# Optimization experiments

Hardware: AMD Instinct MI355X
Metric: run time of the kernel (lower is better)

The kernel has to match this reference:

```python
import jax, jax.numpy as jnp
import numpy as np

NU, NI = 100000, 50000          # users, items
N = NU + NI                      # total nodes
E0 = 1200000                     # directed user->item interactions
B = 100000                       # query (user,item) pairs
D = 64                           # embedding_dim
H1, H2, H3 = 128, 128, 64        # hidden_dims


def setup_inputs() -> dict:
    key = jax.random.key(0)
    ks = jax.random.split(key, 20)
    # bipartite edges, made symmetric (as create_graph does)
    u = jax.random.randint(ks[0], (E0,), 0, NU, dtype=jnp.int32)
    it = jax.random.randint(ks[1], (E0,), NU, N, dtype=jnp.int32)
    src = jnp.concatenate([u, it])   # [2*E0]
    dst = jnp.concatenate([it, u])   # [2*E0]
    user_idx = jax.random.randint(ks[2], (B,), 0, NU, dtype=jnp.int32)
    item_idx = jax.random.randint(ks[3], (B,), 0, NI, dtype=jnp.int32)

    def w(k, shape, fan_in):
        return jax.random.normal(k, shape, jnp.float32) * (1.0 / np.sqrt(fan_in))

    return {
        "user_table": jax.random.normal(ks[4], (NU, D), jnp.float32),
        "item_table": jax.random.normal(ks[5], (NI, D), jnp.float32),
        "W1": w(ks[6], (D, H1), D),   "b1": jnp.zeros((H1,), jnp.float32),
        "W2": w(ks[7], (H1, H2), H1), "b2": jnp.zeros((H2,), jnp.float32),
        "W3": w(ks[8], (H2, H3), H2), "b3": jnp.zeros((H3,), jnp.float32),
        "P1": w(ks[9], (2 * H3, 64), 2 * H3), "pb1": jnp.zeros((64,), jnp.float32),
        "P2": w(ks[10], (64, 32), 64),        "pb2": jnp.zeros((32,), jnp.float32),
        "P3": w(ks[11], (32, 1), 32),         "pb3": jnp.zeros((1,), jnp.float32),
        "src": src, "dst": dst,
        "user_idx": user_idx, "item_idx": item_idx,
    }


def _gconv(x, src, dst, deg_rsqrt, W, b):
    # DGL GraphConv, norm='both': D^{-1/2} A D^{-1/2} X W + b
    h = x * deg_rsqrt[:, None]                              # [N, d]
    m = jax.ops.segment_sum(h[src], dst, num_segments=N)    # gather-scatter over edges
    return (m * deg_rsqrt[:, None]) @ W + b


def reference(user_table, item_table, W1, b1, W2, b2, W3, b3,
              P1, pb1, P2, pb2, P3, pb3, src, dst, user_idx, item_idx):
    # symmetric graph -> in-degree == out-degree
    deg = jax.ops.segment_sum(jnp.ones_like(dst, jnp.float32), dst, num_segments=N)
    deg_rsqrt = jax.lax.rsqrt(jnp.maximum(deg, 1.0))

    x = jnp.concatenate([user_table, item_table], axis=0)   # [N, D]
    x = jax.nn.relu(_gconv(x, src, dst, deg_rsqrt, W1, b1))
    x = jax.nn.relu(_gconv(x, src, dst, deg_rsqrt, W2, b2))
    x = _gconv(x, src, dst, deg_rsqrt, W3, b3)               # [N, H3]

    u = x[user_idx]                                          # [B, H3]
    v = x[NU + item_idx]                                     # [B, H3]
    z = jnp.concatenate([u, v], axis=1)                      # [B, 2*H3]
    z = jax.nn.relu(z @ P1 + pb1)
    z = jax.nn.relu(z @ P2 + pb2)
    return jax.nn.sigmoid(z @ P3 + pb3)                      # [B, 1]
```

## Files before the change

kernel.cpp:

```cpp
#include <hip/hip_runtime.h>
#include <hip/hip_bf16.h>


typedef unsigned short u16;
typedef unsigned int   u32;
typedef __attribute__((ext_vector_type(8))) short short8;
typedef __attribute__((ext_vector_type(4))) float f32x4;

__device__ __forceinline__ float b2f(u16 u){
  union { u32 i; float f; } c; c.i = ((u32)u) << 16; return c.f;
}
__device__ __forceinline__ u16 f2b(float f){
  union { float f; u32 i; } c; c.f = f;
  u32 x = c.i;
  u32 r = x + 0x7FFFu + ((x >> 16) & 1u);
  return (u16)(r >> 16);
}

__device__ __forceinline__ void acc8(uint4 u, float* a){
  a[0] += b2f((u16)(u.x & 0xffff)); a[1] += b2f((u16)(u.x >> 16));
  a[2] += b2f((u16)(u.y & 0xffff)); a[3] += b2f((u16)(u.y >> 16));
  a[4] += b2f((u16)(u.z & 0xffff)); a[5] += b2f((u16)(u.z >> 16));
  a[6] += b2f((u16)(u.w & 0xffff)); a[7] += b2f((u16)(u.w >> 16));
}

#define NWT 43008


__global__ __launch_bounds__(256) void k_histK(const int* __restrict__ dst, int ne, int K,
    u32* __restrict__ bhist,
    const float* __restrict__ W1, const float* __restrict__ W2, const float* __restrict__ W3,
    const float* __restrict__ P1, const float* __restrict__ P2, u16* __restrict__ WT){
  extern __shared__ u32 sh[];
  int t = threadIdx.x;
  for (int i = blockIdx.x*256 + t; i < NWT; i += gridDim.x*256){
    float v;
    if (i < 8192)      { int j=i;        v = W1[(j%64)*128 + j/64];   }
    else if (i < 24576){ int j=i-8192;   v = W2[(j%128)*128 + j/128]; }
    else if (i < 32768){ int j=i-24576;  v = W3[(j%128)*64 + j/128];  }
    else if (i < 40960){ int j=i-32768;  v = P1[(j%128)*64 + j/128];  }
    else               { int j=i-40960;  v = P2[(j%64)*32 + j/64];    }
    WT[i] = f2b(v);
  }
  for (int i = t; i < K; i += 256) sh[i] = 0;
  __syncthreads();
  for (int i = blockIdx.x*256 + t; i < ne; i += gridDim.x*256)
    atomicAdd(&sh[dst[i] >> 8], 1u);
  __syncthreads();
  int rot = (int)((blockIdx.x * 73u) % (u32)K);
  for (int jj = t; jj < K; jj += 256){
    int i = jj + rot; if (i >= K) i -= K;
    u32 v = sh[i];
    if (v) atomicAdd(&bhist[i], v);
  }
}

__global__ __launch_bounds__(256) void k_scanK(const u32* __restrict__ bhist, int K,
                                               u32* __restrict__ bbase, u32* __restrict__ gcur){
  __shared__ u32 s[256];
  int t = threadIdx.x;
  int items = (K + 255) / 256;
  u32 local[16];
  int s0 = t * items;
  u32 sum = 0;
  for (int j = 0; j < items; j++){
    int idx = s0 + j;
    u32 v = (idx < K) ? bhist[idx] : 0;
    local[j] = v; sum += v;
  }
  s[t] = sum; __syncthreads();
  for (int off = 1; off < 256; off <<= 1){
    u32 add = (t >= off) ? s[t-off] : 0;
    __syncthreads();
    s[t] += add;
    __syncthreads();
  }
  u32 run = s[t] - sum;
  for (int j = 0; j < items; j++){
    int idx = s0 + j;
    if (idx < K){ bbase[idx] = run; gcur[idx] = run; }
    run += local[j];
  }
  if (t == 255) bbase[K] = s[255];
}

__global__ __launch_bounds__(256) void k_scatterR(const int* __restrict__ src, const int* __restrict__ dst,
                                                  int ne, int K, u32* __restrict__ gcur,
                                                  u32* __restrict__ ebuf){
  extern __shared__ u32 cnt[];
  int t = threadIdx.x;
  int e0 = blockIdx.x * 4096;
  for (int i = t; i < K; i += 256) cnt[i] = 0;
  __syncthreads();
#pragma unroll
  for (int j = 0; j < 16; j++){
    int e = e0 + j*256 + t;
    if (e < ne) atomicAdd(&cnt[dst[e] >> 8], 1u);
  }
  __syncthreads();
  int rot = (int)((blockIdx.x * 73u) % (u32)K);
  for (int jj = t; jj < K; jj += 256){
    int i = jj + rot; if (i >= K) i -= K;
    u32 c = cnt[i];
    if (c) cnt[i] = atomicAdd(&gcur[i], c);
  }
  __syncthreads();
#pragma unroll
  for (int j = 0; j < 16; j++){
    int e = e0 + j*256 + t;
    if (e < ne){
      int d = dst[e];
      u32 p = atomicAdd(&cnt[d >> 8], 1u);
      ebuf[p] = ((u32)(d & 255) << 18) | (u32)src[e];
    }
  }
}

__global__ __launch_bounds__(256) void k_csr(const u32* __restrict__ ebuf, const u32* __restrict__ bbase,
                                             int n, int ne, int* __restrict__ row_ptr,
                                             float* __restrict__ r, int* __restrict__ col,
                                             const float* __restrict__ ut, const float* __restrict__ it,
                                             int nu, u16* __restrict__ x0){
  __shared__ u32 cnt[256];
  __shared__ u32 pfx[256];
  __shared__ u32 cur[256];
  __shared__ float rsh[256];
  int b = blockIdx.x, t = threadIdx.x;
  u32 bb = bbase[b], be = bbase[b+1];
  int nbase = b << 8;
  int nn = n - nbase; if (nn > 256) nn = 256;
  cnt[t] = 0;
  __syncthreads();
  for (u32 e = bb + t; e < be; e += 256)
    atomicAdd(&cnt[ebuf[e] >> 18], 1u);
  __syncthreads();
  pfx[t] = cnt[t];
  __syncthreads();
  for (int off = 1; off < 256; off <<= 1){
    u32 add = (t >= off) ? pfx[t-off] : 0;
    __syncthreads();
    pfx[t] += add;
    __syncthreads();
  }
  u32 excl = pfx[t] - cnt[t];
  cur[t] = bb + excl;
  if (t < nn){
    float rv = rsqrtf(fmaxf((float)cnt[t], 1.0f));
    row_ptr[nbase + t] = (int)(bb + excl);
    r[nbase + t] = rv;
    rsh[t] = rv;
  }
  __syncthreads();
  for (u32 e = bb + t; e < be; e += 256){
    u32 v = ebuf[e];
    u32 p = atomicAdd(&cur[v >> 18], 1u);
    col[p] = (int)(v & 0x3FFFFu);
  }
  if (b == 0 && t == 0) row_ptr[n] = ne;
  for (int i = t; i < nn*16; i += 256){
    int ln = i >> 4;
    int node = nbase + ln;
    int c4 = (i & 15) << 2;
    float rv = rsh[ln];
    const float* srcp = (node < nu) ? (ut + (size_t)node*64 + c4)
                                    : (it + (size_t)(node-nu)*64 + c4);
    float4 v = *(const float4*)srcp;
    ushort4 o;
    o.x = f2b(v.x*rv); o.y = f2b(v.y*rv); o.z = f2b(v.z*rv); o.w = f2b(v.w*rv);
    *(ushort4*)(x0 + (size_t)node*64 + c4) = o;
  }
}

template<int D, bool BIAS>
__global__ __launch_bounds__(256) void k_agg(const u16* __restrict__ x, const float* __restrict__ r,
    const int* __restrict__ row_ptr, const int* __restrict__ col,
    const float* __restrict__ bias, u16* __restrict__ out, int n){
  constexpr int G = D/8;
  constexpr int E = 64/G;
  int wid = (blockIdx.x*256 + threadIdx.x) >> 6;
  int lane = threadIdx.x & 63;
  if (wid >= n) return;
  int gidx = lane / G;
  int l    = lane % G;
  int beg = row_ptr[wid], end = row_ptr[wid+1];
  float a[8] = {0.f,0.f,0.f,0.f,0.f,0.f,0.f,0.f};
  int e = beg + gidx;
  for (; e + E < end; e += 2*E){
    int s0 = col[e];
    int s1 = col[e+E];
    uint4 u0 = *(const uint4*)(x + (size_t)s0*D + l*8);
    uint4 u1 = *(const uint4*)(x + (size_t)s1*D + l*8);
    acc8(u0, a);
    acc8(u1, a);
  }
  if (e < end){
    int s = col[e];
    acc8(*(const uint4*)(x + (size_t)s*D + l*8), a);
  }
#pragma unroll
  for (int off = G; off < 64; off <<= 1){
#pragma unroll
    for (int i = 0; i < 8; i++) a[i] += __shfl_xor(a[i], off);
  }
  if (gidx == 0){
    float rn = r[wid];
    float v[8];
#pragma unroll
    for (int i = 0; i < 8; i++){
      float y = a[i] * rn;
      if constexpr (BIAS) y += bias[l*8 + i];
      v[i] = y;
    }
    uint4 o;
    o.x = (u32)f2b(v[0]) | ((u32)f2b(v[1]) << 16);
    o.y = (u32)f2b(v[2]) | ((u32)f2b(v[3]) << 16);
    o.z = (u32)f2b(v[4]) | ((u32)f2b(v[5]) << 16);
    o.w = (u32)f2b(v[6]) | ((u32)f2b(v[7]) << 16);
    *(uint4*)(out + (size_t)wid*D + l*8) = o;
  }
}

template<int K_, int OUT, bool BIAS, bool RELU, bool SCALE>
__global__ __launch_bounds__(256) void k_mgemm(
    const u16* __restrict__ A, const u16* __restrict__ WT, const float* __restrict__ bias,
    const float* __restrict__ rr, u16* __restrict__ C, int nrows)
{
  constexpr int NT = OUT / 16;
  constexpr int KS = K_ / 32;
  const int t = threadIdx.x;
  const int wave = t >> 6, lane = t & 63;
  const int quad = lane >> 4, m16 = lane & 15;
  const int rowb = blockIdx.x*128 + wave*32;

  const short8 zz = {0,0,0,0,0,0,0,0};
  short8 afr[2][KS];
#pragma unroll
  for (int mt = 0; mt < 2; mt++){
    int row = rowb + mt*16 + m16;
    bool ok = row < nrows;
#pragma unroll
    for (int ks = 0; ks < KS; ks++){
      afr[mt][ks] = ok ? *(const short8*)(A + (size_t)row*K_ + ks*32 + quad*8) : zz;
    }
  }

  f32x4 acc[2][NT];
#pragma unroll
  for (int mt = 0; mt < 2; mt++)
#pragma unroll
    for (int nt = 0; nt < NT; nt++) acc[mt][nt] = (f32x4){0.f,0.f,0.f,0.f};

#pragma unroll
  for (int nt = 0; nt < NT; nt++){
#pragma unroll
    for (int ks = 0; ks < KS; ks++){
      short8 b = *(const short8*)(WT + (size_t)(nt*16 + m16)*K_ + ks*32 + quad*8);
      acc[0][nt] = __builtin_amdgcn_mfma_f32_16x16x32_bf16(afr[0][ks], b, acc[0][nt], 0, 0, 0);
      acc[1][nt] = __builtin_amdgcn_mfma_f32_16x16x32_bf16(afr[1][ks], b, acc[1][nt], 0, 0, 0);
    }
  }

  float bv[NT];
#pragma unroll
  for (int nt = 0; nt < NT; nt++){
    if constexpr (BIAS) bv[nt] = bias[nt*16 + m16]; else bv[nt] = 0.f;
  }
#pragma unroll
  for (int mt = 0; mt < 2; mt++){
    int row0 = rowb + mt*16 + quad*4;
#pragma unroll
    for (int reg = 0; reg < 4; reg++){
      int row = row0 + reg;
      if (row >= nrows) continue;
      float rs = 1.f;
      if constexpr (SCALE) rs = rr[row];
#pragma unroll
      for (int nt = 0; nt < NT; nt++){
        float v = acc[mt][nt][reg];
        if constexpr (BIAS) v += bv[nt];
        if constexpr (RELU) v = fmaxf(v, 0.f);
        if constexpr (SCALE) v *= rs;
        C[(size_t)row*OUT + nt*16 + m16] = f2b(v);
      }
    }
  }
}

__global__ __launch_bounds__(256) void k_mlp(
    const u16* __restrict__ x3, const u16* __restrict__ WT4, const float* __restrict__ pb1v,
    const u16* __restrict__ WT5, const float* __restrict__ pb2v,
    const float* __restrict__ P3, const float* __restrict__ pb3,
    const int* __restrict__ uidx, const int* __restrict__ vidx,
    int B, int nu, float* __restrict__ outp)
{
  __shared__ u16 a1[128*72];
  const int t = threadIdx.x;
  const int wave = t >> 6, lane = t & 63;
  const int quad = lane >> 4, m16 = lane & 15;
  const int rowb = blockIdx.x*128 + wave*32;

  const short8 zz = {0,0,0,0,0,0,0,0};
  short8 afr[2][4];
#pragma unroll
  for (int mt = 0; mt < 2; mt++){
    int row = rowb + mt*16 + m16;
    bool ok = row < B;
#pragma unroll
    for (int ks = 0; ks < 4; ks++){
      int k = ks*32 + quad*8;
      if (!ok){ afr[mt][ks] = zz; continue; }
      int node, kk;
      if (k < 64){ node = uidx[row];      kk = k; }
      else       { node = nu + vidx[row]; kk = k - 64; }
      afr[mt][ks] = *(const short8*)(x3 + (size_t)node*64 + kk);
    }
  }
  f32x4 acc[2][4];
#pragma unroll
  for (int mt = 0; mt < 2; mt++)
#pragma unroll
    for (int nt = 0; nt < 4; nt++) acc[mt][nt] = (f32x4){0.f,0.f,0.f,0.f};
#pragma unroll
  for (int nt = 0; nt < 4; nt++){
#pragma unroll
    for (int ks = 0; ks < 4; ks++){
      short8 b = *(const short8*)(WT4 + (size_t)(nt*16 + m16)*128 + ks*32 + quad*8);
      acc[0][nt] = __builtin_amdgcn_mfma_f32_16x16x32_bf16(afr[0][ks], b, acc[0][nt], 0, 0, 0);
      acc[1][nt] = __builtin_amdgcn_mfma_f32_16x16x32_bf16(afr[1][ks], b, acc[1][nt], 0, 0, 0);
    }
  }
  float pb1s[4];
#pragma unroll
  for (int nt = 0; nt < 4; nt++) pb1s[nt] = pb1v[nt*16 + m16];
#pragma unroll
  for (int mt = 0; mt < 2; mt++){
    int rl0 = wave*32 + mt*16 + quad*4;
#pragma unroll
    for (int reg = 0; reg < 4; reg++){
#pragma unroll
      for (int nt = 0; nt < 4; nt++){
        float v = fmaxf(acc[mt][nt][reg] + pb1s[nt], 0.f);
        a1[(rl0 + reg)*72 + nt*16 + m16] = f2b(v);
      }
    }
  }
  __syncthreads();

  short8 af2[2][2];
#pragma unroll
  for (int mt = 0; mt < 2; mt++){
    int rl = wave*32 + mt*16 + m16;
#pragma unroll
    for (int ks = 0; ks < 2; ks++)
      af2[mt][ks] = *(const short8*)(a1 + rl*72 + ks*32 + quad*8);
  }
  f32x4 acc2[2][2];
#pragma unroll
  for (int mt = 0; mt < 2; mt++)
#pragma unroll
    for (int nt = 0; nt < 2; nt++) acc2[mt][nt] = (f32x4){0.f,0.f,0.f,0.f};
#pragma unroll
  for (int nt = 0; nt < 2; nt++){
#pragma unroll
    for (int ks = 0; ks < 2; ks++){
      short8 b = *(const short8*)(WT5 + (size_t)(nt*16 + m16)*64 + ks*32 + quad*8);
      acc2[0][nt] = __builtin_amdgcn_mfma_f32_16x16x32_bf16(af2[0][ks], b, acc2[0][nt], 0, 0, 0);
      acc2[1][nt] = __builtin_amdgcn_mfma_f32_16x16x32_bf16(af2[1][ks], b, acc2[1][nt], 0, 0, 0);
    }
  }
  float b0 = pb2v[m16], b1v = pb2v[16 + m16];
  float p0 = P3[m16],   p1 = P3[16 + m16];
  float pb = pb3[0];
#pragma unroll
  for (int mt = 0; mt < 2; mt++){
    float v4[4];
#pragma unroll
    for (int reg = 0; reg < 4; reg++){
      float part = fmaxf(acc2[mt][0][reg] + b0, 0.f) * p0
                 + fmaxf(acc2[mt][1][reg] + b1v, 0.f) * p1;
      part += __shfl_xor(part, 1);
      part += __shfl_xor(part, 2);
      part += __shfl_xor(part, 4);
      part += __shfl_xor(part, 8);
      v4[reg] = 1.f / (1.f + __expf(-(part + pb)));
    }
    if (m16 == 0){
      int row0 = rowb + mt*16 + quad*4;
      if (row0 + 3 < B){
        *(float4*)(outp + row0) = make_float4(v4[0], v4[1], v4[2], v4[3]);
      } else {
#pragma unroll
        for (int reg = 0; reg < 4; reg++)
          if (row0 + reg < B) outp[row0 + reg] = v4[reg];
      }
    }
  }
}


extern "C" void kernel_launch(void* const* d_in, const int* in_sizes, int n_in,
                              void* d_out, int out_size, void* d_ws, size_t ws_size,
                              hipStream_t stream){
  const float* ut  = (const float*)d_in[0];
  const float* it  = (const float*)d_in[1];
  const float* W1  = (const float*)d_in[2];
  const float* b1  = (const float*)d_in[3];
  const float* W2  = (const float*)d_in[4];
  const float* b2  = (const float*)d_in[5];
  const float* W3  = (const float*)d_in[6];
  const float* b3  = (const float*)d_in[7];
  const float* P1  = (const float*)d_in[8];
  const float* pb1 = (const float*)d_in[9];
  const float* P2  = (const float*)d_in[10];
  const float* pb2 = (const float*)d_in[11];
  const float* P3  = (const float*)d_in[12];
  const float* pb3 = (const float*)d_in[13];
  const int* src  = (const int*)d_in[14];
  const int* dst  = (const int*)d_in[15];
  const int* uidx = (const int*)d_in[16];
  const int* vidx = (const int*)d_in[17];

  const int NU = in_sizes[0] / 64;
  const int NI = in_sizes[1] / 64;
  const int N  = NU + NI;
  const int NE = in_sizes[14];
  const int B  = in_sizes[16];
  const int K  = (N + 255) >> 8;

  char* w = (char*)d_ws;
  auto alloc = [&](size_t bytes)->void*{
    void* p = (void*)w;
    w += (bytes + 255) & ~(size_t)255;
    return p;
  };
  float* r       = (float*)alloc((size_t)N*4);
  int*   row_ptr = (int*)  alloc((size_t)(N+1)*4);
  u32*   bhist   = (u32*)  alloc((size_t)K*4);
  u32*   bbase   = (u32*)  alloc((size_t)(K+1)*4);
  u32*   gcur    = (u32*)  alloc((size_t)K*4);
  int*   col     = (int*)  alloc((size_t)NE*4);
  u16*   Wall    = (u16*)  alloc((size_t)NWT*2);
  char*  bufE    = (char*) alloc((size_t)N*64*2 > (size_t)NE*4 ? (size_t)N*64*2 : (size_t)NE*4);
  char*  bufF    = (char*) alloc((size_t)N*128*2);
  u16*   bufC    = (u16*)  alloc((size_t)N*128*2);
  u16*   bufD    = (u16*)  alloc((size_t)N*64*2);
  if ((size_t)(w - (char*)d_ws) > ws_size) return;

  u16* WT1 = Wall;
  u16* WT2 = Wall + 8192;
  u16* WT3 = Wall + 24576;
  u16* WT4 = Wall + 32768;
  u16* WT5 = Wall + 40960;

  u32* ebuf = (u32*)bufE;
  u16* x0   = bufD;

  hipMemsetAsync(bhist, 0, (size_t)K*4, stream);

  int g;
  k_histK  <<<128, 256, (size_t)K*4, stream>>>(dst, NE, K, bhist, W1, W2, W3, P1, P2, Wall);
  k_scanK  <<<1, 256, 0, stream>>>(bhist, K, bbase, gcur);
  g = (NE + 4095)/4096;
  k_scatterR<<<g, 256, (size_t)K*4, stream>>>(src, dst, NE, K, gcur, ebuf);
  k_csr    <<<K, 256, 0, stream>>>(ebuf, bbase, N, NE, row_ptr, r, col, ut, it, NU, x0);

  const int ga  = (N + 3)/4;
  const int gN  = (N + 127)/128;
  const int gB  = (B + 127)/128;

  u16* m1 = (u16*)bufE;
  k_agg<64,false><<<ga,256,0,stream>>>(x0, r, row_ptr, col, nullptr, m1, N);
  u16* h1 = bufC;
  k_mgemm<64,128,true,true,true><<<gN,256,0,stream>>>(m1, WT1, b1, r, h1, N);

  u16* m2 = (u16*)bufF;
  k_agg<128,false><<<ga,256,0,stream>>>(h1, r, row_ptr, col, nullptr, m2, N);
  u16* h2 = bufC;
  k_mgemm<128,128,true,true,true><<<gN,256,0,stream>>>(m2, WT2, b2, r, h2, N);

  u16* g3 = bufD;
  k_mgemm<128,64,false,false,false><<<gN,256,0,stream>>>(h2, WT3, nullptr, nullptr, g3, N);

  u16* x3 = (u16*)bufE;
  k_agg<64,true><<<ga,256,0,stream>>>(g3, r, row_ptr, col, b3, x3, N);

  k_mlp<<<gB,256,0,stream>>>(x3, WT4, pb1, WT5, pb2, P3, pb3, uidx, vidx, B, NU, (float*)d_out);
}
```

Baseline: 510.3 us.

## Fuse neighbor aggregation with MFMA GEMM for first two GCN layers

Adds a k_aggemm kernel in which each wave aggregates 16 nodes' neighbor features into LDS, then multiplies that tile by the layer weight with MFMA, applying bias, ReLU and degree scaling in the same kernel. This removes the round trip of the aggregated m1/m2 buffers through global memory and two kernel launches. Weights are now pre-packed in MFMA fragment order so B-operand loads are contiguous per lane. A now-redundant block barrier in the MLP kernel is dropped, since each wave reads only the LDS rows it wrote. The trade-off is that each wave walks 16 nodes one after another, so fewer independent waves are issuing gathers, which may cut memory-level parallelism in the latency-bound edge gather.

```diff
diff --git a/kernel.cpp b/kernel.cpp
--- a/kernel.cpp
+++ b/kernel.cpp
@@ -26,21 +26,30 @@
 
 #define NWT 43008
 
+__device__ __forceinline__ float wb_src(int i, int KS, int N, const float* W){
+  int frag = i >> 9, rem = i & 511;
+  int lane = rem >> 3, j = rem & 7;
+  int nt = frag / KS, ks = frag % KS;
+  int n = nt*16 + (lane & 15);
+  int k = ks*32 + (lane >> 4)*8 + j;
+  return W[k*N + n];
+}
+
 
 __global__ __launch_bounds__(256) void k_histK(const int* __restrict__ dst, int ne, int K,
     u32* __restrict__ bhist,
     const float* __restrict__ W1, const float* __restrict__ W2, const float* __restrict__ W3,
-    const float* __restrict__ P1, const float* __restrict__ P2, u16* __restrict__ WT){
+    const float* __restrict__ P1, const float* __restrict__ P2, u16* __restrict__ WB){
   extern __shared__ u32 sh[];
   int t = threadIdx.x;
   for (int i = blockIdx.x*256 + t; i < NWT; i += gridDim.x*256){
     float v;
-    if (i < 8192)      { int j=i;        v = W1[(j%64)*128 + j/64];   }
-    else if (i < 24576){ int j=i-8192;   v = W2[(j%128)*128 + j/128]; }
-    else if (i < 32768){ int j=i-24576;  v = W3[(j%128)*64 + j/128];  }
-    else if (i < 40960){ int j=i-32768;  v = P1[(j%128)*64 + j/128];  }
-    else               { int j=i-40960;  v = P2[(j%64)*32 + j/64];    }
-    WT[i] = f2b(v);
+    if (i < 8192)       v = wb_src(i,        2, 128, W1);
+    else if (i < 24576) v = wb_src(i-8192,   4, 128, W2);
+    else if (i < 32768) v = wb_src(i-24576,  4,  64, W3);
+    else if (i < 40960) v = wb_src(i-32768,  4,  64, P1);
+    else                v = wb_src(i-40960,  2,  32, P2);
+    WB[i] = f2b(v);
   }
   for (int i = t; i < K; i += 256) sh[i] = 0;
   __syncthreads();
@@ -168,6 +177,91 @@
     ushort4 o;
     o.x = f2b(v.x*rv); o.y = f2b(v.y*rv); o.z = f2b(v.z*rv); o.w = f2b(v.w*rv);
     *(ushort4*)(x0 + (size_t)node*64 + c4) = o;
+  }
+}
+
+template<int DIN>
+__global__ __launch_bounds__(256) void k_aggemm(
+    const u16* __restrict__ x, const float* __restrict__ r,
+    const int* __restrict__ row_ptr, const int* __restrict__ col,
+    const u16* __restrict__ WB, const float* __restrict__ bias,
+    u16* __restrict__ C, int n)
+{
+  constexpr int G  = DIN/8;
+  constexpr int E  = 64/G;
+  constexpr int KP = DIN + 8;
+  constexpr int KS = DIN/32;
+  __shared__ u16 As[64*KP];
+  const int t = threadIdx.x;
+  const int wave = t >> 6, lane = t & 63;
+  const int gidx = lane / G, l = lane % G;
+  const int quad = lane >> 4, m16 = lane & 15;
+  const int nodeb = blockIdx.x*64 + wave*16;
+
+  for (int i = 0; i < 16; i++){
+    int node = nodeb + i;
+    float a[8] = {0.f,0.f,0.f,0.f,0.f,0.f,0.f,0.f};
+    if (node < n){
+      int beg = row_ptr[node], end = row_ptr[node+1];
+      int e = beg + gidx;
+      for (; e + E < end; e += 2*E){
+        int s0 = col[e];
+        int s1 = col[e+E];
+        uint4 u0 = *(const uint4*)(x + (size_t)s0*DIN + l*8);
+        uint4 u1 = *(const uint4*)(x + (size_t)s1*DIN + l*8);
+        acc8(u0, a);
+        acc8(u1, a);
+      }
+      if (e < end) acc8(*(const uint4*)(x + (size_t)col[e]*DIN + l*8), a);
+    }
+#pragma unroll
+    for (int off = G; off < 64; off <<= 1){
+#pragma unroll
+      for (int j = 0; j < 8; j++) a[j] += __shfl_xor(a[j], off);
+    }
+    if (gidx == 0){
+      float rn = (node < n) ? r[node] : 0.f;
+      uint4 o;
+      o.x = (u32)f2b(a[0]*rn) | ((u32)f2b(a[1]*rn) << 16);
+      o.y = (u32)f2b(a[2]*rn) | ((u32)f2b(a[3]*rn) << 16);
+      o.z = (u32)f2b(a[4]*rn) | ((u32)f2b(a[5]*rn) << 16);
+      o.w = (u32)f2b(a[6]*rn) | ((u32)f2b(a[7]*rn) << 16);
+      *(uint4*)(As + (size_t)(wave*16 + i)*KP + l*8) = o;
+    }
+  }
+
+  short8 afr[KS];
+#pragma unroll
+  for (int ks = 0; ks < KS; ks++)
+    afr[ks] = *(const short8*)(As + (size_t)(wave*16 + m16)*KP + ks*32 + quad*8);
+
+  f32x4 acc[8];
+#pragma unroll
+  for (int nt = 0; nt < 8; nt++) acc[nt] = (f32x4){0.f,0.f,0.f,0.f};
+#pragma unroll
+  for (int nt = 0; nt < 8; nt++){
+#pragma unroll
+    for (int ks = 0; ks < KS; ks++){
+      short8 b = *(const short8*)(WB + (size_t)((nt*KS + ks)*64 + lane)*8);
+      acc[nt] = __builtin_amdgcn_mfma_f32_16x16x32_bf16(afr[ks], b, acc[nt], 0, 0, 0);
+    }
+  }
+
+  float bv[8];
+#pragma unroll
+  for (int nt = 0; nt < 8; nt++) bv[nt] = bias[nt*16 + m16];
+  int row0 = nodeb + quad*4;
+#pragma unroll
+  for (int reg = 0; reg < 4; reg++){
+    int row = row0 + reg;
+    if (row < n){
+      float rs = r[row];
+#pragma unroll
+      for (int nt = 0; nt < 8; nt++){
+        float v = fmaxf(acc[nt][reg] + bv[nt], 0.f) * rs;
+        C[(size_t)row*128 + nt*16 + m16] = f2b(v);
+      }
+    }
   }
 }
 
@@ -194,8 +288,7 @@
     acc8(u1, a);
   }
   if (e < end){
-    int s = col[e];
-    acc8(*(const uint4*)(x + (size_t)s*D + l*8), a);
+    acc8(*(const uint4*)(x + (size_t)col[e]*D + l*8), a);
   }
 #pragma unroll
   for (int off = G; off < 64; off <<= 1){
@@ -220,50 +313,37 @@
   }
 }
 
-template<int K_, int OUT, bool BIAS, bool RELU, bool SCALE>
-__global__ __launch_bounds__(256) void k_mgemm(
-    const u16* __restrict__ A, const u16* __restrict__ WT, const float* __restrict__ bias,
-    const float* __restrict__ rr, u16* __restrict__ C, int nrows)
+__global__ __launch_bounds__(256) void k_gemm3(
+    const u16* __restrict__ A, const u16* __restrict__ WB, u16* __restrict__ C, int nrows)
 {
-  constexpr int NT = OUT / 16;
-  constexpr int KS = K_ / 32;
   const int t = threadIdx.x;
   const int wave = t >> 6, lane = t & 63;
   const int quad = lane >> 4, m16 = lane & 15;
   const int rowb = blockIdx.x*128 + wave*32;
 
   const short8 zz = {0,0,0,0,0,0,0,0};
-  short8 afr[2][KS];
+  short8 afr[2][4];
 #pragma unroll
   for (int mt = 0; mt < 2; mt++){
     int row = rowb + mt*16 + m16;
     bool ok = row < nrows;
 #pragma unroll
-    for (int ks = 0; ks < KS; ks++){
-      afr[mt][ks] = ok ? *(const short8*)(A + (size_t)row*K_ + ks*32 + quad*8) : zz;
-    }
-  }
-
-  f32x4 acc[2][NT];
+    for (int ks = 0; ks < 4; ks++)
+      afr[mt][ks] = ok ? *(const short8*)(A + (size_t)row*128 + ks*32 + quad*8) : zz;
+  }
+  f32x4 acc[2][4];
 #pragma unroll
   for (int mt = 0; mt < 2; mt++)
 #pragma unroll
-    for (int nt = 0; nt < NT; nt++) acc[mt][nt] = (f32x4){0.f,0.f,0.f,0.f};
-
-#pragma unroll
-  for (int nt = 0; nt < NT; nt++){
-#pragma unroll
-    for (int ks = 0; ks < KS; ks++){
-      short8 b = *(const short8*)(WT + (size_t)(nt*16 + m16)*K_ + ks*32 + quad*8);
+    for (int nt = 0; nt < 4; nt++) acc[mt][nt] = (f32x4){0.f,0.f,0.f,0.f};
+#pragma unroll
+  for (int nt = 0; nt < 4; nt++){
+#pragma unroll
+    for (int ks = 0; ks < 4; ks++){
+      short8 b = *(const short8*)(WB + (size_t)((nt*4 + ks)*64 + lane)*8);
       acc[0][nt] = __builtin_amdgcn_mfma_f32_16x16x32_bf16(afr[0][ks], b, acc[0][nt], 0, 0, 0);
       acc[1][nt] = __builtin_amdgcn_mfma_f32_16x16x32_bf16(afr[1][ks], b, acc[1][nt], 0, 0, 0);
     }
-  }
-
-  float bv[NT];
-#pragma unroll
-  for (int nt = 0; nt < NT; nt++){
-    if constexpr (BIAS) bv[nt] = bias[nt*16 + m16]; else bv[nt] = 0.f;
   }
 #pragma unroll
   for (int mt = 0; mt < 2; mt++){
@@ -272,23 +352,16 @@
     for (int reg = 0; reg < 4; reg++){
       int row = row0 + reg;
       if (row >= nrows) continue;
-      float rs = 1.f;
-      if constexpr (SCALE) rs = rr[row];
-#pragma unroll
-      for (int nt = 0; nt < NT; nt++){
-        float v = acc[mt][nt][reg];
-        if constexpr (BIAS) v += bv[nt];
-        if constexpr (RELU) v = fmaxf(v, 0.f);
-        if constexpr (SCALE) v *= rs;
-        C[(size_t)row*OUT + nt*16 + m16] = f2b(v);
-      }
+#pragma unroll
+      for (int nt = 0; nt < 4; nt++)
+        C[(size_t)row*64 + nt*16 + m16] = f2b(acc[mt][nt][reg]);
     }
   }
 }
 
 __global__ __launch_bounds__(256) void k_mlp(
-    const u16* __restrict__ x3, const u16* __restrict__ WT4, const float* __restrict__ pb1v,
-    const u16* __restrict__ WT5, const float* __restrict__ pb2v,
+    const u16* __restrict__ x3, const u16* __restrict__ WB4, const float* __restrict__ pb1v,
+    const u16* __restrict__ WB5, const float* __restrict__ pb2v,
     const float* __restrict__ P3, const float* __restrict__ pb3,
     const int* __restrict__ uidx, const int* __restrict__ vidx,
     int B, int nu, float* __restrict__ outp)
@@ -324,7 +397,7 @@
   for (int nt = 0; nt < 4; nt++){
 #pragma unroll
     for (int ks = 0; ks < 4; ks++){
-      short8 b = *(const short8*)(WT4 + (size_t)(nt*16 + m16)*128 + ks*32 + quad*8);
+      short8 b = *(const short8*)(WB4 + (size_t)((nt*4 + ks)*64 + lane)*8);
       acc[0][nt] = __builtin_amdgcn_mfma_f32_16x16x32_bf16(afr[0][ks], b, acc[0][nt], 0, 0, 0);
       acc[1][nt] = __builtin_amdgcn_mfma_f32_16x16x32_bf16(afr[1][ks], b, acc[1][nt], 0, 0, 0);
     }
@@ -344,8 +417,6 @@
       }
     }
   }
-  __syncthreads();
-
   short8 af2[2][2];
 #pragma unroll
   for (int mt = 0; mt < 2; mt++){
@@ -363,7 +434,7 @@
   for (int nt = 0; nt < 2; nt++){
 #pragma unroll
     for (int ks = 0; ks < 2; ks++){
-      short8 b = *(const short8*)(WT5 + (size_t)(nt*16 + m16)*64 + ks*32 + quad*8);
+      short8 b = *(const short8*)(WB5 + (size_t)((nt*2 + ks)*64 + lane)*8);
       acc2[0][nt] = __builtin_amdgcn_mfma_f32_16x16x32_bf16(af2[0][ks], b, acc2[0][nt], 0, 0, 0);
       acc2[1][nt] = __builtin_amdgcn_mfma_f32_16x16x32_bf16(af2[1][ks], b, acc2[1][nt], 0, 0, 0);
     }
@@ -446,11 +517,11 @@
   u16*   bufD    = (u16*)  alloc((size_t)N*64*2);
   if ((size_t)(w - (char*)d_ws) > ws_size) return;
 
-  u16* WT1 = Wall;
-  u16* WT2 = Wall + 8192;
-  u16* WT3 = Wall + 24576;
-  u16* WT4 = Wall + 32768;
-  u16* WT5 = Wall + 40960;
+  u16* WB1 = Wall;
+  u16* WB2 = Wall + 8192;
+  u16* WB3 = Wall + 24576;
+  u16* WB4 = Wall + 32768;
+  u16* WB5 = Wall + 40960;
 
   u32* ebuf = (u32*)bufE;
   u16* x0   = bufD;
@@ -464,25 +535,22 @@
   k_scatterR<<<g, 256, (size_t)K*4, stream>>>(src, dst, NE, K, gcur, ebuf);
   k_csr    <<<K, 256, 0, stream>>>(ebuf, bbase, N, NE, row_ptr, r, col, ut, it, NU, x0);
 
+  const int gA  = (N + 63)/64;
   const int ga  = (N + 3)/4;
   const int gN  = (N + 127)/128;
   const int gB  = (B + 127)/128;
 
-  u16* m1 = (u16*)bufE;
-  k_agg<64,false><<<ga,256,0,stream>>>(x0, r, row_ptr, col, nullptr, m1, N);
   u16* h1 = bufC;
-  k_mgemm<64,128,true,true,true><<<gN,256,0,stream>>>(m1, WT1, b1, r, h1, N);
-
-  u16* m2 = (u16*)bufF;
-  k_agg<128,false><<<ga,256,0,stream>>>(h1, r, row_ptr, col, nullptr, m2, N);
-  u16* h2 = bufC;
-  k_mgemm<128,128,true,true,true><<<gN,256,0,stream>>>(m2, WT2, b2, r, h2, N);
+  k_aggemm<64><<<gA,256,0,stream>>>(x0, r, row_ptr, col, WB1, b1, h1, N);
+
+  u16* h2 = (u16*)bufF;
+  k_aggemm<128><<<gA,256,0,stream>>>(h1, r, row_ptr, col, WB2, b2, h2, N);
 
   u16* g3 = bufD;
-  k_mgemm<128,64,false,false,false><<<gN,256,0,stream>>>(h2, WT3, nullptr, nullptr, g3, N);
+  k_gemm3<<<gN,256,0,stream>>>(h2, WB3, g3, N);
 
   u16* x3 = (u16*)bufE;
   k_agg<64,true><<<ga,256,0,stream>>>(g3, r, row_ptr, col, b3, x3, N);
 
-  k_mlp<<<gB,256,0,stream>>>(x3, WT4, pb1, WT5, pb2, P3, pb3, uidx, vidx, B, NU, (float*)d_out);
-}
+  k_mlp<<<gB,256,0,stream>>>(x3, WB4, pb1, WB5, pb2, P3, pb3, uidx, vidx, B, NU, (float*)d_out);
+}
```

Result: slower. 523.9 us (+2.7%).
